# Kernel tuning notes

Measured on AMD Instinct MI355X. Metric: run time of the kernel, lower is better.

## Reference

```python
import jax, jax.numpy as jnp
import numpy as np

N = 100000   # nodes
E = 640000   # edges
D = 128      # in_channels
C = 40       # out_channels (classes)


def setup_inputs() -> dict:
    key = jax.random.key(0)
    ks = jax.random.split(key, 6)
    x = jax.random.normal(ks[0], (N, D), jnp.float32)
    edge_index = jax.random.randint(ks[1], (2, E), 0, N)
    edge_weight = jax.random.uniform(ks[2], (E,), jnp.float32)
    # 8 block convs (4 blocks x 2) stacked, + final conv
    Wb = jax.random.normal(ks[3], (8, D, D), jnp.float32) / np.sqrt(D)
    bb = jnp.zeros((8, D), jnp.float32)
    Wf = jax.random.normal(ks[4], (D, C), jnp.float32) / np.sqrt(D)
    bf = jnp.zeros((C,), jnp.float32)
    return dict(x=x, edge_index=edge_index, edge_weight=edge_weight,
                Wb=Wb, bb=bb, Wf=Wf, bf=bf)


def _gcn(x, W, b, src, dst, w):
    """PyG GCNConv (normalize=True) with self-loops already appended to src/dst/w."""
    n = x.shape[0]
    h = x @ W                                   # [N, out]
    deg = jax.ops.segment_sum(w, dst, num_segments=n)
    dinv = jnp.where(deg > 0, jax.lax.rsqrt(deg), 0.0)
    norm = dinv[src] * w * dinv[dst]            # [E+N]
    out = jax.ops.segment_sum(h[src] * norm[:, None], dst, num_segments=n)
    return out + b


def reference(x, edge_index, edge_weight, Wb, bb, Wf, bf):
    n = x.shape[0]
    loop = jnp.arange(n)
    src = jnp.concatenate([edge_index[0], loop])
    dst = jnp.concatenate([edge_index[1], loop])
    w = jnp.concatenate([edge_weight, jnp.ones((n,), x.dtype)])
    # forward only runs blocks 1-4 (blocks 5-7 unused in the original forward)
    for i in range(4):
        identity = x
        x = jax.nn.relu(_gcn(x, Wb[2 * i], bb[2 * i], src, dst, w))
        # dropout: identity in eval mode
        x = jax.nn.relu(_gcn(x, Wb[2 * i + 1], bb[2 * i + 1], src, dst, w))
        # F.normalize: row-wise L2 with eps=1e-12
        x = x / jnp.maximum(jnp.linalg.norm(x, axis=1, keepdims=True), 1e-12)
        x = (x + identity) / 2
    x = _gcn(x, Wf, bf, src, dst, w)
    return jax.nn.log_softmax(x, axis=1)
```

## Files before the change

kernel.cpp:

```cpp
#include <hip/hip_runtime.h>
#include <math.h>

#define NN 100000
#define EE 640000
#define DD 128
#define CC 40
#define FIXS 4194304.0f

typedef __bf16 bf16x8 __attribute__((ext_vector_type(8)));
typedef float f32x4 __attribute__((ext_vector_type(4)));
typedef unsigned short us8 __attribute__((ext_vector_type(8)));

__device__ inline unsigned short f2b(float f) {
    union { float f; unsigned u; } v; v.f = f;
    unsigned u = v.u;
    return (unsigned short)((u + 0x7FFFu + ((u >> 16) & 1u)) >> 16);
}
__device__ inline float b2f(unsigned short b) {
    union { unsigned u; float f; } v; v.u = ((unsigned)b) << 16;
    return v.f;
}


__global__ __launch_bounds__(256) void k_edge1(const int* __restrict__ dst,
                                               const float* __restrict__ w,
                                               unsigned long long* __restrict__ degcnt,
                                               int* __restrict__ pos) {
    int e = blockIdx.x * 256 + threadIdx.x;
    if (e < EE) {
        int d = dst[e];
        unsigned long long pk =
            ((unsigned long long)(unsigned)(w[e] * FIXS) << 32) | 1ull;
        unsigned long long old = atomicAdd(&degcnt[d], pk);
        pos[e] = (int)(old & 0xffffffffull);
    }
}

__global__ __launch_bounds__(256) void k_scan1p(const unsigned long long* __restrict__ degcnt,
                                                float* __restrict__ dinv,
                                                int* __restrict__ out,
                                                int* __restrict__ partial,
                                                const float* __restrict__ Wb,
                                                const float* __restrict__ Wf,
                                                unsigned short* __restrict__ WT,
                                                unsigned short* __restrict__ WfT) {
    int t = threadIdx.x;
    if (blockIdx.x >= 98) {
        int idx = (blockIdx.x - 98) * 256 + t;
        if (idx < 8 * DD * DD) {
            int m = idx >> 14;
            int n = (idx >> 7) & 127;
            int k = idx & 127;
            WT[idx] = f2b(Wb[(size_t)m * DD * DD + (size_t)k * DD + n]);
        } else {
            int j = idx - 8 * DD * DD;
            if (j < 64 * DD) {
                int n = j >> 7;
                int k = j & 127;
                WfT[j] = (n < CC) ? f2b(Wf[(size_t)k * CC + n]) : 0;
            }
        }
        return;
    }
    __shared__ int lds[256];
    int base = blockIdx.x * 1024 + t * 4;
    int v[4]; int s = 0;
    #pragma unroll
    for (int j = 0; j < 4; ++j) {
        int idx = base + j;
        unsigned long long dc = (idx < NN) ? degcnt[idx] : 0ull;
        v[j] = (int)(dc & 0xffffffffull);
        s += v[j];
        if (idx < NN)
            dinv[idx] = rsqrtf((float)(unsigned)(dc >> 32) * (1.0f / FIXS) + 1.0f);
    }
    lds[t] = s;
    __syncthreads();
    for (int off = 1; off < 256; off <<= 1) {
        int x = lds[t];
        int y = (t >= off) ? lds[t - off] : 0;
        __syncthreads();
        lds[t] = x + y;
        __syncthreads();
    }
    int excl = lds[t] - s;
    if (t == 255) partial[blockIdx.x] = lds[255];
    int run = excl;
    #pragma unroll
    for (int j = 0; j < 4; ++j) {
        int idx = base + j;
        if (idx < NN) out[idx] = run;
        run += v[j];
    }
}

__global__ __launch_bounds__(256) void k_scan3(int* __restrict__ rp,
                                               const int* __restrict__ partial) {
    __shared__ int lds[128];
    int t = threadIdx.x;
    if (t < 128) lds[t] = (t < 98) ? partial[t] : 0;
    __syncthreads();
    for (int off = 1; off < 128; off <<= 1) {
        int x = (t < 128) ? lds[t] : 0;
        int y = (t >= off && t < 128) ? lds[t - off] : 0;
        __syncthreads();
        if (t < 128) lds[t] = x + y;
        __syncthreads();
    }
    int i = blockIdx.x * 256 + t;
    if (i < NN) {
        int c = i >> 10;
        int add = c ? lds[c - 1] : 0;
        rp[i] += add;
    }
    if (i == 0) rp[NN] = EE;
}

__global__ __launch_bounds__(256) void k_scatter(const int* __restrict__ src,
                                                 const int* __restrict__ dst,
                                                 const float* __restrict__ w,
                                                 const float* __restrict__ dinv,
                                                 const int* __restrict__ rp,
                                                 const int* __restrict__ pos,
                                                 int2* __restrict__ cvp) {
    int e = blockIdx.x * 256 + threadIdx.x;
    if (e < EE) {
        int s = src[e], d = dst[e];
        int p = rp[d] + pos[e];
        int2 cv;
        cv.x = s;
        cv.y = __float_as_int(dinv[s] * w[e] * dinv[d]);
        cvp[p] = cv;
    }
}

__global__ __launch_bounds__(256) void k_x2bf(const float* __restrict__ x,
                                              unsigned short* __restrict__ Abf) {
    int idx = blockIdx.x * 256 + threadIdx.x;
    if (idx >= NN * DD / 4) return;
    float4 v = ((const float4*)x)[idx];
    ushort4 r;
    r.x = f2b(v.x); r.y = f2b(v.y); r.z = f2b(v.z); r.w = f2b(v.w);
    ((ushort4*)Abf)[idx] = r;
}


#define MM_EPILOGUE_128(H_)                                                  \
    {                                                                        \
        _Pragma("unroll")                                                    \
        for (int n = 0; n < 8; ++n) {                                        \
            _Pragma("unroll")                                                \
            for (int v = 0; v < 4; ++v)                                      \
                tb[wid][g * 4 + v][n * 16 + sl] = f2b(acc[n][v]);            \
        }                                                                    \
        _Pragma("unroll")                                                    \
        for (int c4 = 0; c4 < 4; ++c4) {                                     \
            int chunk = c4 * 64 + lane;                                      \
            int row = chunk >> 4, seg = chunk & 15;                          \
            int grow = r0 + row;                                             \
            if (grow < NN)                                                   \
                *(us8*)(H_ + (size_t)grow * DD + seg * 8) =                  \
                    *(const us8*)(&tb[wid][row][seg * 8]);                   \
        }                                                                    \
    }

__global__ __launch_bounds__(256) void k_mm_mfma(const unsigned short* __restrict__ X,
                                                 const unsigned short* __restrict__ WT,
                                                 unsigned short* __restrict__ H) {
    __shared__ unsigned short tb[4][16][136];
    int wid = threadIdx.x >> 6;
    int lane = threadIdx.x & 63;
    int r0 = blockIdx.x * 64 + wid * 16;
    int sl = lane & 15, g = lane >> 4;
    int arow = r0 + sl;
    if (arow >= NN) arow = NN - 1;

    f32x4 acc[8];
    #pragma unroll
    for (int n = 0; n < 8; ++n) acc[n] = (f32x4){0.f, 0.f, 0.f, 0.f};

    const bf16x8* xrow = (const bf16x8*)(X + (size_t)arow * DD);
    #pragma unroll
    for (int kc = 0; kc < 4; ++kc) {
        bf16x8 a = xrow[kc * 4 + g];
        #pragma unroll
        for (int n = 0; n < 8; ++n) {
            const bf16x8* wrow = (const bf16x8*)(WT + (size_t)(n * 16 + sl) * DD);
            bf16x8 b = wrow[kc * 4 + g];
            acc[n] = __builtin_amdgcn_mfma_f32_16x16x32_bf16(a, b, acc[n], 0, 0, 0);
        }
    }
    MM_EPILOGUE_128(H);
}

__global__ __launch_bounds__(256) void k_mm40b(const unsigned short* __restrict__ X,
                                               const unsigned short* __restrict__ WfT,
                                               unsigned short* __restrict__ H) {
    __shared__ unsigned short tb[4][16][72];
    int wid = threadIdx.x >> 6;
    int lane = threadIdx.x & 63;
    int r0 = blockIdx.x * 64 + wid * 16;
    int sl = lane & 15, g = lane >> 4;
    int arow = r0 + sl;
    if (arow >= NN) arow = NN - 1;

    f32x4 acc[4];
    #pragma unroll
    for (int n = 0; n < 4; ++n) acc[n] = (f32x4){0.f, 0.f, 0.f, 0.f};

    const bf16x8* xrow = (const bf16x8*)(X + (size_t)arow * DD);
    #pragma unroll
    for (int kc = 0; kc < 4; ++kc) {
        bf16x8 a = xrow[kc * 4 + g];
        #pragma unroll
        for (int n = 0; n < 4; ++n) {
            const bf16x8* wrow = (const bf16x8*)(WfT + (size_t)(n * 16 + sl) * DD);
            bf16x8 b = wrow[kc * 4 + g];
            acc[n] = __builtin_amdgcn_mfma_f32_16x16x32_bf16(a, b, acc[n], 0, 0, 0);
        }
    }
    #pragma unroll
    for (int n = 0; n < 4; ++n) {
        #pragma unroll
        for (int v = 0; v < 4; ++v)
            tb[wid][g * 4 + v][n * 16 + sl] = f2b(acc[n][v]);
    }
    #pragma unroll
    for (int c4 = 0; c4 < 2; ++c4) {
        int chunk = c4 * 64 + lane;
        int row = chunk >> 3, seg = chunk & 7;
        int grow = r0 + row;
        if (grow < NN)
            *(us8*)(H + (size_t)grow * 64 + seg * 8) =
                *(const us8*)(&tb[wid][row][seg * 8]);
    }
}


#define AGG_CORE(h_, node_, sl_, a_, STRIDE_)                               \
    {                                                                       \
        float dv = dinv[node_];                                             \
        float dv2 = dv * dv;                                                \
        us8 m_ = ((const us8*)(h_ + (size_t)node_ * STRIDE_))[sl_];         \
        _Pragma("unroll")                                                   \
        for (int j = 0; j < 8; ++j) a_[j] = dv2 * b2f(m_[j]);               \
        int e = rp[node_], end = rp[node_ + 1];                             \
        for (; e + 4 <= end; e += 4) {                                      \
            int2 c0 = cvp[e], c1 = cvp[e + 1], c2 = cvp[e + 2], c3 = cvp[e + 3]; \
            us8 q0 = ((const us8*)(h_ + (size_t)c0.x * STRIDE_))[sl_];      \
            us8 q1 = ((const us8*)(h_ + (size_t)c1.x * STRIDE_))[sl_];      \
            us8 q2 = ((const us8*)(h_ + (size_t)c2.x * STRIDE_))[sl_];      \
            us8 q3 = ((const us8*)(h_ + (size_t)c3.x * STRIDE_))[sl_];      \
            float v0 = __int_as_float(c0.y), v1 = __int_as_float(c1.y);     \
            float v2 = __int_as_float(c2.y), v3 = __int_as_float(c3.y);     \
            _Pragma("unroll")                                               \
            for (int j = 0; j < 8; ++j)                                     \
                a_[j] += (v0 * b2f(q0[j]) + v1 * b2f(q1[j]))                \
                       + (v2 * b2f(q2[j]) + v3 * b2f(q3[j]));               \
        }                                                                   \
        for (; e < end; ++e) {                                              \
            int2 c0 = cvp[e];                                               \
            us8 q0 = ((const us8*)(h_ + (size_t)c0.x * STRIDE_))[sl_];      \
            float v0 = __int_as_float(c0.y);                                \
            _Pragma("unroll")                                               \
            for (int j = 0; j < 8; ++j) a_[j] += v0 * b2f(q0[j]);           \
        }                                                                   \
    }

__global__ __launch_bounds__(256) void k_agg128(const unsigned short* __restrict__ h,
                                                const float* __restrict__ dinv,
                                                const int* __restrict__ rp,
                                                const int2* __restrict__ cvp,
                                                const float* __restrict__ bias,
                                                unsigned short* __restrict__ outb) {
    int node = blockIdx.x * 16 + (threadIdx.x >> 4);
    int sl = threadIdx.x & 15;
    if (node >= NN) return;
    float a[8];
    AGG_CORE(h, node, sl, a, DD);
    float4 bz0 = ((const float4*)bias)[sl * 2];
    float4 bz1 = ((const float4*)bias)[sl * 2 + 1];
    float bb[8] = {bz0.x, bz0.y, bz0.z, bz0.w, bz1.x, bz1.y, bz1.z, bz1.w};
    us8 r;
    #pragma unroll
    for (int j = 0; j < 8; ++j) r[j] = f2b(fmaxf(a[j] + bb[j], 0.f));
    ((us8*)(outb + (size_t)node * DD))[sl] = r;
}

__global__ __launch_bounds__(256) void k_agg128_nr(const unsigned short* __restrict__ h,
                                                   const float* __restrict__ dinv,
                                                   const int* __restrict__ rp,
                                                   const int2* __restrict__ cvp,
                                                   const float* __restrict__ bias,
                                                   unsigned short* __restrict__ Abf) {
    int node = blockIdx.x * 16 + (threadIdx.x >> 4);
    int sl = threadIdx.x & 15;
    if (node >= NN) return;
    float a[8];
    AGG_CORE(h, node, sl, a, DD);
    float4 bz0 = ((const float4*)bias)[sl * 2];
    float4 bz1 = ((const float4*)bias)[sl * 2 + 1];
    float bb[8] = {bz0.x, bz0.y, bz0.z, bz0.w, bz1.x, bz1.y, bz1.z, bz1.w};
    float ss = 0.f;
    #pragma unroll
    for (int j = 0; j < 8; ++j) {
        a[j] = fmaxf(a[j] + bb[j], 0.f);
        ss += a[j] * a[j];
    }
    ss += __shfl_xor(ss, 1);
    ss += __shfl_xor(ss, 2);
    ss += __shfl_xor(ss, 4);
    ss += __shfl_xor(ss, 8);
    float sc = 1.0f / fmaxf(sqrtf(ss), 1e-12f);
    us8 oldb = ((const us8*)(Abf + (size_t)node * DD))[sl];
    us8 rb;
    #pragma unroll
    for (int j = 0; j < 8; ++j)
        rb[j] = f2b((a[j] * sc + b2f(oldb[j])) * 0.5f);
    ((us8*)(Abf + (size_t)node * DD))[sl] = rb;
}

__global__ __launch_bounds__(256) void k_agg_final(const unsigned short* __restrict__ h,
                                                   const float* __restrict__ dinv,
                                                   const int* __restrict__ rp,
                                                   const int2* __restrict__ cvp,
                                                   const float* __restrict__ bias,
                                                   float* __restrict__ out) {
    int node = blockIdx.x * 32 + (threadIdx.x >> 3);
    int sl = threadIdx.x & 7;
    if (node >= NN) return;
    float a[8];
    AGG_CORE(h, node, sl, a, 64);
    bool real = sl < 5;
    float vv[8];
    if (real) {
        float4 bz0 = ((const float4*)bias)[sl * 2];
        float4 bz1 = ((const float4*)bias)[sl * 2 + 1];
        float bb[8] = {bz0.x, bz0.y, bz0.z, bz0.w, bz1.x, bz1.y, bz1.z, bz1.w};
        #pragma unroll
        for (int j = 0; j < 8; ++j) vv[j] = a[j] + bb[j];
    } else {
        #pragma unroll
        for (int j = 0; j < 8; ++j) vv[j] = -3.0e38f;
    }
    float m = vv[0];
    #pragma unroll
    for (int j = 1; j < 8; ++j) m = fmaxf(m, vv[j]);
    m = fmaxf(m, __shfl_xor(m, 1));
    m = fmaxf(m, __shfl_xor(m, 2));
    m = fmaxf(m, __shfl_xor(m, 4));
    float s = 0.f;
    if (real) {
        #pragma unroll
        for (int j = 0; j < 8; ++j) s += expf(vv[j] - m);
    }
    s += __shfl_xor(s, 1);
    s += __shfl_xor(s, 2);
    s += __shfl_xor(s, 4);
    float ls = m + logf(s);
    if (real) {
        float4 o0 = {vv[0] - ls, vv[1] - ls, vv[2] - ls, vv[3] - ls};
        float4 o1 = {vv[4] - ls, vv[5] - ls, vv[6] - ls, vv[7] - ls};
        float* orow = out + (size_t)node * CC + sl * 8;
        *(float4*)(orow) = o0;
        *(float4*)(orow + 4) = o1;
    }
}


extern "C" void kernel_launch(void* const* d_in, const int* in_sizes, int n_in,
                              void* d_out, int out_size, void* d_ws, size_t ws_size,
                              hipStream_t stream) {
    const float* x  = (const float*)d_in[0];
    const int*   ei = (const int*)d_in[1];
    const float* ew = (const float*)d_in[2];
    const float* Wb = (const float*)d_in[3];
    const float* bb = (const float*)d_in[4];
    const float* Wf = (const float*)d_in[5];
    const float* bf_ = (const float*)d_in[6];
    const int* src = ei;
    const int* dst = ei + EE;
    float* out = (float*)d_out;

    char* p = (char*)d_ws;
    unsigned short*     Abf    = (unsigned short*)p;     p += (size_t)NN * DD * 2;
    unsigned short*     Bbf    = (unsigned short*)p;     p += (size_t)NN * DD * 2;
    unsigned short*     Cbf    = (unsigned short*)p;     p += (size_t)NN * DD * 2;
    unsigned short*     H48    = (unsigned short*)p;     p += (size_t)NN * 64 * 2;
    unsigned short*     WT     = (unsigned short*)p;     p += (size_t)8 * DD * DD * 2;
    unsigned short*     WfT    = (unsigned short*)p;     p += (size_t)64 * DD * 2;
    unsigned long long* degcnt = (unsigned long long*)p; p += (size_t)NN * 8;
    float* dinv = (float*)p; p += (size_t)NN * 4;
    int*   rp   = (int*)p;   p += (size_t)(NN + 1) * 4;
    int*   pos  = (int*)p;   p += (size_t)EE * 4;
    int2*  cvp  = (int2*)p;  p += (size_t)EE * 8;
    int*   partial = (int*)p; p += 128 * 4;

    hipMemsetAsync(degcnt, 0, (size_t)NN * 8, stream);

    k_edge1<<<(EE + 255) / 256, 256, 0, stream>>>(dst, ew, degcnt, pos);
    k_scan1p<<<98 + (8 * DD * DD + 64 * DD + 255) / 256, 256, 0, stream>>>(
        degcnt, dinv, rp, partial, Wb, Wf, WT, WfT);
    k_scan3<<<(NN + 255) / 256, 256, 0, stream>>>(rp, partial);
    k_scatter<<<(EE + 255) / 256, 256, 0, stream>>>(src, dst, ew, dinv, rp, pos, cvp);
    k_x2bf<<<(NN * DD / 4 + 255) / 256, 256, 0, stream>>>(x, Abf);

    int gb = (NN + 63) / 64;
    k_mm_mfma<<<gb, 256, 0, stream>>>(Abf, WT, Bbf);
    for (int blk = 0; blk < 4; ++blk) {
        k_agg128<<<(NN + 15) / 16, 256, 0, stream>>>(Bbf, dinv, rp, cvp,
                                                     bb + (size_t)(2 * blk) * DD, Cbf);
        k_mm_mfma<<<gb, 256, 0, stream>>>(Cbf, WT + (size_t)(2 * blk + 1) * DD * DD, Bbf);
        k_agg128_nr<<<(NN + 15) / 16, 256, 0, stream>>>(Bbf, dinv, rp, cvp,
                                                        bb + (size_t)(2 * blk + 1) * DD, Abf);
        if (blk < 3)
            k_mm_mfma<<<gb, 256, 0, stream>>>(Abf, WT + (size_t)(2 * blk + 2) * DD * DD, Bbf);
    }
    k_mm40b<<<gb, 256, 0, stream>>>(Abf, WfT, H48);
    k_agg_final<<<(NN + 31) / 32, 256, 0, stream>>>(H48, dinv, rp, cvp, bf_, out);
}
```

Before: 646.3 us.

## Sort nodes by in-degree bucket to balance aggregation wavefronts

Adds a degree histogram, a prefix scan and a scatter pass that build a node permutation grouped by in-degree (capped at 31). All aggregation kernels now process nodes in that order, so the node groups sharing a wavefront have similar edge-loop lengths and less divergence. The cost is three extra small launches and scattered row writes in place of the previous sequential ones.

```diff
diff --git a/kernel.cpp b/kernel.cpp
--- a/kernel.cpp
+++ b/kernel.cpp
@@ -34,6 +34,52 @@
         unsigned long long old = atomicAdd(&degcnt[d], pk);
         pos[e] = (int)(old & 0xffffffffull);
     }
+}
+
+
+__global__ __launch_bounds__(256) void k_dhist(const unsigned long long* __restrict__ degcnt,
+                                               int* __restrict__ gbin) {
+    __shared__ int lh[32];
+    int t = threadIdx.x;
+    if (t < 32) lh[t] = 0;
+    __syncthreads();
+    int i = blockIdx.x * 256 + t;
+    if (i < NN) {
+        int d = (int)(degcnt[i] & 0xffffffffull);
+        d = d < 31 ? d : 31;
+        atomicAdd(&lh[d], 1);
+    }
+    __syncthreads();
+    if (t < 32 && lh[t]) atomicAdd(&gbin[t], lh[t]);
+}
+
+__global__ __launch_bounds__(64) void k_dscan(int* __restrict__ gbin) {
+    if (threadIdx.x == 0) {
+        int run = 0;
+        for (int b = 0; b < 32; ++b) { int c = gbin[b]; gbin[b] = run; run += c; }
+    }
+}
+
+__global__ __launch_bounds__(256) void k_dscatter(const unsigned long long* __restrict__ degcnt,
+                                                  int* __restrict__ gbin,
+                                                  int* __restrict__ order) {
+    __shared__ int lh[32];
+    __shared__ int lbase[32];
+    int t = threadIdx.x;
+    if (t < 32) lh[t] = 0;
+    __syncthreads();
+    int i = blockIdx.x * 256 + t;
+    int d = 0, r = 0;
+    bool ok = i < NN;
+    if (ok) {
+        d = (int)(degcnt[i] & 0xffffffffull);
+        d = d < 31 ? d : 31;
+        r = atomicAdd(&lh[d], 1);
+    }
+    __syncthreads();
+    if (t < 32) lbase[t] = lh[t] ? atomicAdd(&gbin[32 + t], lh[t]) : 0;
+    __syncthreads();
+    if (ok) order[gbin[d] + lbase[d] + r] = i;
 }
 
 __global__ __launch_bounds__(256) void k_scan1p(const unsigned long long* __restrict__ degcnt,
@@ -271,11 +317,13 @@
                                                 const float* __restrict__ dinv,
                                                 const int* __restrict__ rp,
                                                 const int2* __restrict__ cvp,
+                                                const int* __restrict__ order,
                                                 const float* __restrict__ bias,
                                                 unsigned short* __restrict__ outb) {
-    int node = blockIdx.x * 16 + (threadIdx.x >> 4);
+    int slot = blockIdx.x * 16 + (threadIdx.x >> 4);
     int sl = threadIdx.x & 15;
-    if (node >= NN) return;
+    if (slot >= NN) return;
+    int node = order[slot];
     float a[8];
     AGG_CORE(h, node, sl, a, DD);
     float4 bz0 = ((const float4*)bias)[sl * 2];
@@ -291,11 +339,13 @@
                                                    const float* __restrict__ dinv,
                                                    const int* __restrict__ rp,
                                                    const int2* __restrict__ cvp,
+                                                   const int* __restrict__ order,
                                                    const float* __restrict__ bias,
                                                    unsigned short* __restrict__ Abf) {
-    int node = blockIdx.x * 16 + (threadIdx.x >> 4);
+    int slot = blockIdx.x * 16 + (threadIdx.x >> 4);
     int sl = threadIdx.x & 15;
-    if (node >= NN) return;
+    if (slot >= NN) return;
+    int node = order[slot];
     float a[8];
     AGG_CORE(h, node, sl, a, DD);
     float4 bz0 = ((const float4*)bias)[sl * 2];
@@ -324,11 +374,13 @@
                                                    const float* __restrict__ dinv,
                                                    const int* __restrict__ rp,
                                                    const int2* __restrict__ cvp,
+                                                   const int* __restrict__ order,
                                                    const float* __restrict__ bias,
                                                    float* __restrict__ out) {
-    int node = blockIdx.x * 32 + (threadIdx.x >> 3);
+    int slot = blockIdx.x * 32 + (threadIdx.x >> 3);
     int sl = threadIdx.x & 7;
-    if (node >= NN) return;
+    if (slot >= NN) return;
+    int node = order[slot];
     float a[8];
     AGG_CORE(h, node, sl, a, 64);
     bool real = sl < 5;
@@ -390,17 +442,22 @@
     unsigned short*     WT     = (unsigned short*)p;     p += (size_t)8 * DD * DD * 2;
     unsigned short*     WfT    = (unsigned short*)p;     p += (size_t)64 * DD * 2;
     unsigned long long* degcnt = (unsigned long long*)p; p += (size_t)NN * 8;
+    int*   gbin = (int*)p;   p += 64 * 4;
     float* dinv = (float*)p; p += (size_t)NN * 4;
     int*   rp   = (int*)p;   p += (size_t)(NN + 1) * 4;
     int*   pos  = (int*)p;   p += (size_t)EE * 4;
     int2*  cvp  = (int2*)p;  p += (size_t)EE * 8;
+    int*   order = (int*)p;  p += (size_t)NN * 4;
     int*   partial = (int*)p; p += 128 * 4;
 
-    hipMemsetAsync(degcnt, 0, (size_t)NN * 8, stream);
+    hipMemsetAsync(degcnt, 0, (size_t)NN * 8 + 64 * 4, stream);
 
     k_edge1<<<(EE + 255) / 256, 256, 0, stream>>>(dst, ew, degcnt, pos);
+    k_dhist<<<(NN + 255) / 256, 256, 0, stream>>>(degcnt, gbin);
     k_scan1p<<<98 + (8 * DD * DD + 64 * DD + 255) / 256, 256, 0, stream>>>(
         degcnt, dinv, rp, partial, Wb, Wf, WT, WfT);
+    k_dscan<<<1, 64, 0, stream>>>(gbin);
+    k_dscatter<<<(NN + 255) / 256, 256, 0, stream>>>(degcnt, gbin, order);
     k_scan3<<<(NN + 255) / 256, 256, 0, stream>>>(rp, partial);
     k_scatter<<<(EE + 255) / 256, 256, 0, stream>>>(src, dst, ew, dinv, rp, pos, cvp);
     k_x2bf<<<(NN * DD / 4 + 255) / 256, 256, 0, stream>>>(x, Abf);
@@ -408,14 +465,14 @@
     int gb = (NN + 63) / 64;
     k_mm_mfma<<<gb, 256, 0, stream>>>(Abf, WT, Bbf);
     for (int blk = 0; blk < 4; ++blk) {
-        k_agg128<<<(NN + 15) / 16, 256, 0, stream>>>(Bbf, dinv, rp, cvp,
+        k_agg128<<<(NN + 15) / 16, 256, 0, stream>>>(Bbf, dinv, rp, cvp, order,
                                                      bb + (size_t)(2 * blk) * DD, Cbf);
         k_mm_mfma<<<gb, 256, 0, stream>>>(Cbf, WT + (size_t)(2 * blk + 1) * DD * DD, Bbf);
-        k_agg128_nr<<<(NN + 15) / 16, 256, 0, stream>>>(Bbf, dinv, rp, cvp,
+        k_agg128_nr<<<(NN + 15) / 16, 256, 0, stream>>>(Bbf, dinv, rp, cvp, order,
                                                         bb + (size_t)(2 * blk + 1) * DD, Abf);
         if (blk < 3)
             k_mm_mfma<<<gb, 256, 0, stream>>>(Abf, WT + (size_t)(2 * blk + 2) * DD * DD, Bbf);
     }
     k_mm40b<<<gb, 256, 0, stream>>>(Abf, WfT, H48);
-    k_agg_final<<<(NN + 31) / 32, 256, 0, stream>>>(H48, dinv, rp, cvp, bf_, out);
-}
+    k_agg_final<<<(NN + 31) / 32, 256, 0, stream>>>(H48, dinv, rp, cvp, order, bf_, out);
+}
```

Result: slower. 674.3 us (+4.3%).
